# Performance work log

Measured on AMD Instinct MI355X. Metric: run time of the kernel, lower is better.

The kernel has to match this reference:

```python
import jax, jax.numpy as jnp
import numpy as np
from jax import lax

jax.config.update("jax_enable_x64", True)

B = 32768          # batch size
NCS = 96           # number of charging stations
NB = 124           # num_buses
S_BASE = 1000.0
MAX_CS = 22.17
MIN_CS = -22.17
MAX_EV_CH = 22.0
MAX_EV_DIS = -22.0
EV_CAP = 70.0
EV_MIN_CAP = 15.0
ITERS = 100
TOL = 1e-06
DT = 15.0 / 60.0   # timescale (hours)


def setup_inputs() -> dict:
    ks = jax.random.split(jax.random.key(0), 12)
    action = jax.random.uniform(ks[0], (B, NCS), dtype=jnp.float32, minval=-1.0, maxval=1.0)
    prices = jax.random.uniform(ks[1], (B, 1), dtype=jnp.float32, minval=0.05, maxval=0.5)
    active = jax.random.uniform(ks[2], (B, NB - 1), dtype=jnp.float32, minval=0.0, maxval=50.0)
    reactive = jax.random.uniform(ks[3], (B, NB - 1), dtype=jnp.float32, minval=0.0, maxval=20.0)
    cap = jax.random.uniform(ks[4], (B, NCS), dtype=jnp.float32, minval=0.0, maxval=EV_CAP)
    cap = cap * (jax.random.uniform(ks[5], (B, NCS)) > 0.2).astype(jnp.float32)
    tleft = jax.random.randint(ks[6], (B, NCS), 1, 10).astype(jnp.float32)
    bus = jax.random.randint(ks[7], (B, NCS), 0, NB - 1).astype(jnp.float32)
    ev = jnp.stack([cap, tleft, bus], axis=-1).reshape(B, 3 * NCS)  # interleaved triples
    state = jnp.concatenate(
        [jnp.zeros((B, 3), jnp.float32), prices, active, reactive, ev], axis=1
    )  # (B, 4 + 2*(NB-1) + 3*NCS) == (B, 538)
    K_re = (0.005 * jax.random.normal(ks[8], (NB - 1, NB - 1))).astype(jnp.float32)
    K_im = (0.005 * jax.random.normal(ks[9], (NB - 1, NB - 1))).astype(jnp.float32)
    L_re = jnp.ones((NB - 1,), jnp.float32)
    L_im = jnp.zeros((NB - 1,), jnp.float32)
    return {"action": action, "state": state, "K_re": K_re, "K_im": K_im, "L_re": L_re, "L_im": L_im}


def _forward(action, state, K_re, K_im, L_re, L_im):
    b, ncs = action.shape
    nb1 = NB - 1
    es = 4 + 2 * nb1  # start of EV state block
    prices = state[:, 3:4]                                    # (B,1), broadcast over stations
    cap = state[:, es:es + 3 * ncs:3]                         # current capacity
    tleft = state[:, es + 1:es + 1 + 3 * ncs:3]               # time left
    bus = state[:, es + 2:es + 2 + 3 * ncs:3].astype(jnp.int32)  # connected bus index
    conn = (cap > 0).astype(action.dtype)
    max_ch = jnp.minimum(MAX_EV_CH, conn * (EV_CAP - cap) / DT)
    max_dis = jnp.maximum(MAX_EV_DIS, conn * (EV_MIN_CAP - cap) / DT)
    pos = jnp.where(action >= 0, 1.0, 0.0).astype(action.dtype)
    power = action * MAX_CS * pos - action * MIN_CS * (1.0 - pos)
    power = jnp.maximum(jnp.minimum(power, max_ch), max_dis)
    costs = (prices * power * DT).sum(axis=1)
    new_cap = jnp.ceil((cap + power * DT) * 100.0) / 100.0
    dep = (tleft == 1).astype(action.dtype)
    user_sat = (-10.0 * dep * (new_cap - EV_CAP) ** 2).sum(axis=1)
    # scatter-add EV power per bus (duplicate indices accumulate, like torch scatter_add)
    ev_bus = jnp.zeros((b, nb1), power.dtype).at[jnp.arange(b)[:, None], bus].add(power)
    ap = state[:, 4:4 + nb1]
    rp = state[:, 4 + nb1:4 + 2 * nb1]
    S = ((ap + ev_bus) / S_BASE + 1j * (rp / S_BASE)).astype(jnp.complex128)  # (B, NB-1)
    K = (K_re + 1j * K_im).astype(jnp.complex128)
    W = (L_re + 1j * L_im).astype(jnp.complex128)
    v_init = jnp.ones((b, nb1), jnp.complex128)

    def run(v0):
        # Z-bus fixed point: v_k = K @ conj(S / v0)^T + W   (batched as bi)
        vk = jnp.einsum('ij,bj->bi', K, jnp.conj(S / v0)) + W
        tol = jnp.max(jnp.abs(jnp.abs(vk) - jnp.abs(v0)))
        return vk, tol

    def body(carry, _):
        v0, done = carry
        def step(v):
            vk, tol = run(v)
            return vk, tol < TOL
        def skip(v):
            return v, jnp.array(True)
        v_next, conv = lax.cond(done, skip, step, v0)
        return (v_next, done | conv), None

    (v_fin, _), _ = lax.scan(body, (v_init, jnp.array(False)), None, length=ITERS)
    vmag = jnp.abs(v_fin)
    voltage_loss = jnp.minimum(0.0, 0.05 - jnp.abs(1.0 - vmag)).sum(axis=1)
    loss = 1000.0 * voltage_loss + costs + user_sat
    return loss.astype(jnp.float32)


def reference(action, state, K_re, K_im, L_re, L_im):
    return _forward(action, state, K_re, K_im, L_re, L_im)
```

## Files before the change

kernel.cpp:

```cpp
#include <hip/hip_runtime.h>

#define NB1   123
#define NCSd  96
#define SW    538
#define EPB   16
#define TPB   256
#define BT    16
#define STPB  128


__global__ __launch_bounds__(128) void k_rowmax(const float* __restrict__ Kre,
                                                const float* __restrict__ Kim,
                                                const float* __restrict__ Lre,
                                                const float* __restrict__ Lim,
                                                float* __restrict__ ws) {
    __shared__ float rmax[2], wmax[2];
    int j = threadIdx.x;
    float s = 0.f, w = 0.f;
    if (j < NB1) {
        for (int k = 0; k < NB1; ++k) {
            float a = Kre[j * NB1 + k], b = Kim[j * NB1 + k];
            s = fmaf(a, a, fmaf(b, b, s));
        }
        float dr = Lre[j] - 1.0f, di = Lim[j];
        w = sqrtf(dr * dr + di * di);
    }
    float r = sqrtf(s);
    #pragma unroll
    for (int off = 32; off; off >>= 1) {
        r = fmaxf(r, __shfl_xor(r, off));
        w = fmaxf(w, __shfl_xor(w, off));
    }
    if ((j & 63) == 0) { rmax[j >> 6] = r; wmax[j >> 6] = w; }
    __syncthreads();
    if (j == 0) {
        ws[0] = fmaxf(rmax[0], rmax[1]);
        ws[2] = fmaxf(wmax[0], wmax[1]);
        ((unsigned*)ws)[1] = 0u;
    }
}

__global__ __launch_bounds__(TPB) void k_fast(const float* __restrict__ action,
                                              const float* __restrict__ state,
                                              float* __restrict__ ws,
                                              float* __restrict__ out) {
    __shared__ float ev[EPB][128];
    const int tid = threadIdx.x;
    const int e = tid >> 4, l = tid & 15;
    const long b = (long)(blockIdx.x * EPB + e);
    const float* srow = state + b * SW;

    for (int k = l; k < 128; k += 16) ev[e][k] = 0.f;
    __syncthreads();

    const float pr = srow[3];
    float costL = 0.f, usatL = 0.f;
    #pragma unroll
    for (int s = 0; s < NCSd / 16; ++s) {
        int i = l + 16 * s;
        float cap = srow[250 + 3 * i];
        float tl  = srow[251 + 3 * i];
        int   bus = (int)srow[252 + 3 * i];
        float a   = action[b * NCSd + i];
        float conn = cap > 0.f ? 1.f : 0.f;
        float mch = fminf(22.0f,  conn * (70.0f - cap) * 4.0f);
        float mds = fmaxf(-22.0f, conn * (15.0f - cap) * 4.0f);
        float p = fmaxf(fminf(22.17f * a, mch), mds);
        costL = fmaf(pr * p, 0.25f, costL);
        float nc = ceilf((cap + p * 0.25f) * 100.0f) * 0.01f;
        if (tl == 1.0f) { float d = nc - 70.0f; usatL = fmaf(-10.0f * d, d, usatL); }
        atomicAdd(&ev[e][bus], p);
    }
    __syncthreads();

    float s2 = 0.f;
    for (int k = l; k < NB1; k += 16) {
        float apv = srow[4 + k] + ev[e][k];
        float rpv = srow[127 + k];
        s2 = fmaf(apv, apv, fmaf(rpv, rpv, s2));
    }
    #pragma unroll
    for (int off = 8; off; off >>= 1) {
        s2    += __shfl_xor(s2, off);
        costL += __shfl_xor(costL, off);
        usatL += __shfl_xor(usatL, off);
    }

    bool flagged = false;
    if (l == 0) {
        float q  = sqrtf(s2) * 0.001f;
        float R  = ws[0];
        float dW = ws[2];
        float x  = R * q * 1.001f + 1e-7f;
        float om = 1.0f - dW;
        float disc = om * om - 4.0f * x;
        bool safe = false;
        if (disc > 0.f) {
            float m = 0.5f * (om + sqrtf(disc));
            safe = (dW + x / m) < 0.0495f;
        }
        flagged = !safe;
        out[b] = costL + usatL;
    }
    unsigned long long mask = __ballot(flagged);
    if (mask) {
        int nf = __popcll(mask);
        int lead = __ffsll((long long)mask) - 1;
        int lane = tid & 63;
        unsigned base_ = 0;
        if (lane == lead) base_ = atomicAdd(((unsigned*)ws) + 1, (unsigned)nf);
        base_ = __shfl(base_, lead);
        if (flagged) {
            int rank = __popcll(mask & ((1ull << lane) - 1ull));
            ((unsigned*)ws)[3 + base_ + rank] = (unsigned)b;
        }
    }
}

__global__ __launch_bounds__(STPB) void k_solve(const float* __restrict__ action,
                                                const float* __restrict__ state,
                                                const float* __restrict__ Kre,
                                                const float* __restrict__ Kim,
                                                const float* __restrict__ Lre,
                                                const float* __restrict__ Lim,
                                                const float* __restrict__ ws,
                                                float* __restrict__ out) {
    __shared__ float ev[BT][STPB];
    __shared__ __align__(16) float2 cmat[STPB][BT + 2];
    __shared__ float vls[STPB][BT + 1];
    __shared__ float red[2];
    __shared__ unsigned idxs[BT];
    const unsigned count = ((const unsigned*)ws)[1];
    const int tid = threadIdx.x;
    const int j = tid;
    const bool jok = j < NB1;
    const float Wre = jok ? Lre[j] : 1.f;
    const float Wim = jok ? Lim[j] : 0.f;

    for (unsigned base = (unsigned)blockIdx.x * BT; base < count; base += (unsigned)gridDim.x * BT) {
        unsigned nv = count - base; if (nv > BT) nv = BT;
        if (tid < BT) {
            unsigned t = (unsigned)tid < nv ? (unsigned)tid : nv - 1;
            idxs[tid] = ((const unsigned*)ws)[3 + base + t];
        }
        for (int x = tid; x < BT * STPB; x += STPB) ((float*)ev)[x] = 0.f;
        __syncthreads();

        for (int task = tid; task < BT * NCSd; task += STPB) {
            int e = task / NCSd, i = task - e * NCSd;
            long b = (long)idxs[e];
            const float* srow = state + b * SW;
            float cap = srow[250 + 3 * i];
            int   bus = (int)srow[252 + 3 * i];
            float a   = action[b * NCSd + i];
            float conn = cap > 0.f ? 1.f : 0.f;
            float mch = fminf(22.0f,  conn * (70.0f - cap) * 4.0f);
            float mds = fmaxf(-22.0f, conn * (15.0f - cap) * 4.0f);
            float p = fmaxf(fminf(22.17f * a, mch), mds);
            atomicAdd(&ev[e][bus], p);
        }
        __syncthreads();

        float Sre[BT], Sim[BT], vr[BT], vi[BT];
        #pragma unroll
        for (int e = 0; e < BT; ++e) {
            long b = (long)idxs[e];
            float ap = jok ? state[b * SW + 4 + j]   : 0.f;
            float rp = jok ? state[b * SW + 127 + j] : 0.f;
            Sre[e] = (ap + ev[e][j]) * 0.001f;
            Sim[e] = rp * 0.001f;
            vr[e] = 1.f; vi[e] = 0.f;
        }
        for (int it = 0; it < 100; ++it) {
            #pragma unroll
            for (int e = 0; e < BT; ++e) {
                float d = vr[e] * vr[e] + vi[e] * vi[e];
                float inv = 1.0f / d;
                cmat[j][e] = make_float2((Sre[e] * vr[e] + Sim[e] * vi[e]) * inv,
                                         (Sre[e] * vi[e] - Sim[e] * vr[e]) * inv);
            }
            __syncthreads();
            float ar[BT], ai[BT];
            #pragma unroll
            for (int e = 0; e < BT; ++e) { ar[e] = Wre; ai[e] = Wim; }
            for (int k = 0; k < NB1; ++k) {
                float kr = jok ? Kre[j * NB1 + k] : 0.f;
                float ki = jok ? Kim[j * NB1 + k] : 0.f;
                const float4* crow = (const float4*)(&cmat[k][0]);
                #pragma unroll
                for (int eh = 0; eh < BT / 2; ++eh) {
                    float4 c2 = crow[eh];
                    ar[2*eh]   = fmaf(kr, c2.x, fmaf(-ki, c2.y, ar[2*eh]));
                    ai[2*eh]   = fmaf(kr, c2.y, fmaf( ki, c2.x, ai[2*eh]));
                    ar[2*eh+1] = fmaf(kr, c2.z, fmaf(-ki, c2.w, ar[2*eh+1]));
                    ai[2*eh+1] = fmaf(kr, c2.w, fmaf( ki, c2.z, ai[2*eh+1]));
                }
            }
            float md = 0.f;
            #pragma unroll
            for (int e = 0; e < BT; ++e) {
                float vmn = sqrtf(ar[e]*ar[e] + ai[e]*ai[e]);
                float vmo = sqrtf(vr[e]*vr[e] + vi[e]*vi[e]);
                md = fmaxf(md, fabsf(vmn - vmo));
                vr[e] = ar[e]; vi[e] = ai[e];
            }
            #pragma unroll
            for (int off = 32; off; off >>= 1) md = fmaxf(md, __shfl_xor(md, off));
            if ((tid & 63) == 0) red[tid >> 6] = md;
            __syncthreads();
            if (fmaxf(red[0], red[1]) < 1e-6f) break;
        }
        #pragma unroll
        for (int e = 0; e < BT; ++e) {
            float vm = sqrtf(vr[e]*vr[e] + vi[e]*vi[e]);
            vls[j][e] = jok ? fminf(0.f, 0.05f - fabsf(1.0f - vm)) : 0.f;
        }
        __syncthreads();
        if (tid < (int)nv) {
            float s = 0.f;
            for (int k = 0; k < NB1; ++k) s += vls[k][tid];
            long b = (long)idxs[tid];
            out[b] += 1000.0f * s;
        }
        __syncthreads();
    }
}

__global__ __launch_bounds__(STPB) void k_main(
    const float* __restrict__ action, const float* __restrict__ state,
    const float* __restrict__ Kre, const float* __restrict__ Kim,
    const float* __restrict__ Lre, const float* __restrict__ Lim,
    float* __restrict__ out)
{
    __shared__ float ev[BT][STPB];
    __shared__ float costs_s[BT];
    __shared__ float usat_s[BT];
    __shared__ __align__(16) float2 cmat[STPB][BT + 2];
    __shared__ float vls[STPB][BT + 1];
    __shared__ float red[2];
    const int tid = threadIdx.x;
    const int e0  = blockIdx.x * BT;
    for (int x = tid; x < BT * STPB; x += STPB) ((float*)ev)[x] = 0.f;
    if (tid < BT) { costs_s[tid] = 0.f; usat_s[tid] = 0.f; }
    __syncthreads();
    for (int task = tid; task < BT * NCSd; task += STPB) {
        int e = task / NCSd, i = task - e * NCSd;
        long b = (long)(e0 + e);
        const float* srow = state + b * SW;
        float cap = srow[250 + 3 * i], tleft = srow[251 + 3 * i];
        int bus = (int)srow[252 + 3 * i];
        float a = action[b * NCSd + i];
        float conn = cap > 0.f ? 1.f : 0.f;
        float mch = fminf(22.0f, conn * (70.0f - cap) * 4.0f);
        float mds = fmaxf(-22.0f, conn * (15.0f - cap) * 4.0f);
        float power = fmaxf(fminf(22.17f * a, mch), mds);
        atomicAdd(&costs_s[e], srow[3] * power * 0.25f);
        float nc = ceilf((cap + power * 0.25f) * 100.0f) * 0.01f;
        if (tleft == 1.0f) { float d = nc - 70.0f; atomicAdd(&usat_s[e], -10.0f * d * d); }
        atomicAdd(&ev[e][bus], power);
    }
    __syncthreads();
    const int j = tid;
    const bool jok = j < NB1;
    float Wre = jok ? Lre[j] : 1.0f, Wim = jok ? Lim[j] : 0.0f;
    float Sre[BT], Sim[BT], vr[BT], vi[BT];
    #pragma unroll
    for (int e = 0; e < BT; ++e) {
        long b = (long)(e0 + e);
        float ap = jok ? state[b * SW + 4 + j] : 0.f;
        float rp = jok ? state[b * SW + 127 + j] : 0.f;
        Sre[e] = (ap + ev[e][j]) * 0.001f; Sim[e] = rp * 0.001f;
        vr[e] = 1.f; vi[e] = 0.f;
    }
    for (int it = 0; it < 100; ++it) {
        #pragma unroll
        for (int e = 0; e < BT; ++e) {
            float d = vr[e]*vr[e] + vi[e]*vi[e];
            float inv = 1.0f / d;
            cmat[j][e] = make_float2((Sre[e]*vr[e] + Sim[e]*vi[e]) * inv,
                                     (Sre[e]*vi[e] - Sim[e]*vr[e]) * inv);
        }
        __syncthreads();
        float ar[BT], ai[BT];
        #pragma unroll
        for (int e = 0; e < BT; ++e) { ar[e] = Wre; ai[e] = Wim; }
        for (int k = 0; k < NB1; ++k) {
            float kr = jok ? Kre[j*NB1+k] : 0.f;
            float ki = jok ? Kim[j*NB1+k] : 0.f;
            const float4* crow = (const float4*)(&cmat[k][0]);
            #pragma unroll
            for (int eh = 0; eh < BT / 2; ++eh) {
                float4 c2 = crow[eh];
                ar[2*eh]   = fmaf(kr, c2.x, fmaf(-ki, c2.y, ar[2*eh]));
                ai[2*eh]   = fmaf(kr, c2.y, fmaf( ki, c2.x, ai[2*eh]));
                ar[2*eh+1] = fmaf(kr, c2.z, fmaf(-ki, c2.w, ar[2*eh+1]));
                ai[2*eh+1] = fmaf(kr, c2.w, fmaf( ki, c2.z, ai[2*eh+1]));
            }
        }
        float md = 0.f;
        #pragma unroll
        for (int e = 0; e < BT; ++e) {
            float vmn = sqrtf(ar[e]*ar[e] + ai[e]*ai[e]);
            float vmo = sqrtf(vr[e]*vr[e] + vi[e]*vi[e]);
            md = fmaxf(md, fabsf(vmn - vmo));
            vr[e] = ar[e]; vi[e] = ai[e];
        }
        #pragma unroll
        for (int off = 32; off > 0; off >>= 1) md = fmaxf(md, __shfl_xor(md, off));
        if ((tid & 63) == 0) red[tid >> 6] = md;
        __syncthreads();
        if (fmaxf(red[0], red[1]) < 1e-6f) break;
    }
    #pragma unroll
    for (int e = 0; e < BT; ++e) {
        float vm = sqrtf(vr[e]*vr[e] + vi[e]*vi[e]);
        vls[j][e] = jok ? fminf(0.f, 0.05f - fabsf(1.0f - vm)) : 0.f;
    }
    __syncthreads();
    if (tid < BT) {
        float s = 0.f;
        for (int k = 0; k < NB1; ++k) s += vls[k][tid];
        out[e0 + tid] = 1000.0f * s + costs_s[tid] + usat_s[tid];
    }
}

extern "C" void kernel_launch(void* const* d_in, const int* in_sizes, int n_in,
                              void* d_out, int out_size, void* d_ws, size_t ws_size,
                              hipStream_t stream) {
    const float* action = (const float*)d_in[0];
    const float* state  = (const float*)d_in[1];
    const float* Kre    = (const float*)d_in[2];
    const float* Kim    = (const float*)d_in[3];
    const float* Lre    = (const float*)d_in[4];
    const float* Lim    = (const float*)d_in[5];
    float* out = (float*)d_out;
    const int B = out_size;

    const size_t wsNeed = (size_t)(3 + B) * sizeof(unsigned);
    if (ws_size >= wsNeed) {
        float* ws = (float*)d_ws;
        hipLaunchKernelGGL(k_rowmax, dim3(1), dim3(128), 0, stream, Kre, Kim, Lre, Lim, ws);
        hipLaunchKernelGGL(k_fast, dim3((B + EPB - 1) / EPB), dim3(TPB), 0, stream,
                           action, state, ws, out);
        hipLaunchKernelGGL(k_solve, dim3(2048), dim3(STPB), 0, stream,
                           action, state, Kre, Kim, Lre, Lim, ws, out);
    } else {
        hipLaunchKernelGGL(k_main, dim3((B + BT - 1) / BT), dim3(STPB), 0, stream,
                           action, state, Kre, Kim, Lre, Lim, out);
    }
}
```

Before: 43.01 us.

## Stage state rows in shared memory, parallelize norm kernel, shrink solve grid

The fast-path kernel now copies each block's 16 state rows into shared memory with coalesced float2 loads, instead of issuing strided per-lane global reads. The row-norm precompute kernel is rewritten so that one wave processes a whole row with shuffle reductions, replacing the serial per-thread loops, and the workspace slot layout is changed to match. The solve kernel's persistent grid is cut from 2048 to 256 blocks, which lowers launch and idle-block overhead when few rows are flagged but gives less parallelism if many rows need the iterative solve. The fast-path grid also drops its ceiling division and now assumes B is a multiple of 16.

Result: slower. 70.90 us (+64.8%).

```diff
diff --git a/kernel.cpp b/kernel.cpp
--- a/kernel.cpp
+++ b/kernel.cpp
@@ -7,36 +7,49 @@
 #define TPB   256
 #define BT    16
 #define STPB  128
-
-
-__global__ __launch_bounds__(128) void k_rowmax(const float* __restrict__ Kre,
-                                                const float* __restrict__ Kim,
-                                                const float* __restrict__ Lre,
-                                                const float* __restrict__ Lim,
-                                                float* __restrict__ ws) {
-    __shared__ float rmax[2], wmax[2];
-    int j = threadIdx.x;
-    float s = 0.f, w = 0.f;
-    if (j < NB1) {
-        for (int k = 0; k < NB1; ++k) {
-            float a = Kre[j * NB1 + k], b = Kim[j * NB1 + k];
-            s = fmaf(a, a, fmaf(b, b, s));
-        }
-        float dr = Lre[j] - 1.0f, di = Lim[j];
-        w = sqrtf(dr * dr + di * di);
-    }
-    float r = sqrtf(s);
-    #pragma unroll
-    for (int off = 32; off; off >>= 1) {
-        r = fmaxf(r, __shfl_xor(r, off));
-        w = fmaxf(w, __shfl_xor(w, off));
-    }
-    if ((j & 63) == 0) { rmax[j >> 6] = r; wmax[j >> 6] = w; }
-    __syncthreads();
-    if (j == 0) {
-        ws[0] = fmaxf(rmax[0], rmax[1]);
-        ws[2] = fmaxf(wmax[0], wmax[1]);
-        ((unsigned*)ws)[1] = 0u;
+#define LROW  540
+
+
+__global__ __launch_bounds__(256) void k_norm(const float* __restrict__ Kre,
+                                              const float* __restrict__ Kim,
+                                              const float* __restrict__ Lre,
+                                              const float* __restrict__ Lim,
+                                              float* __restrict__ ws) {
+    __shared__ float wred[8];
+    const int tid = threadIdx.x;
+    const int w = tid >> 6, l = tid & 63;
+    float rmax2 = 0.f;
+    for (int j = w; j < NB1; j += 4) {
+        const float* kr = Kre + j * NB1;
+        const float* ki = Kim + j * NB1;
+        float a = kr[l], bb = ki[l];
+        float s = fmaf(a, a, bb * bb);
+        if (l + 64 < NB1) {
+            float a2 = kr[l + 64], b2 = ki[l + 64];
+            s = fmaf(a2, a2, fmaf(b2, b2, s));
+        }
+        #pragma unroll
+        for (int off = 32; off; off >>= 1) s += __shfl_xor(s, off);
+        rmax2 = fmaxf(rmax2, s);
+    }
+    float dw2 = 0.f;
+    if (w == 0) {
+        float dr = Lre[l] - 1.f, di = Lim[l];
+        dw2 = fmaf(dr, dr, di * di);
+        if (l + 64 < NB1) {
+            float dr2 = Lre[l + 64] - 1.f, di2 = Lim[l + 64];
+            dw2 = fmaxf(dw2, fmaf(dr2, dr2, di2 * di2));
+        }
+        #pragma unroll
+        for (int off = 32; off; off >>= 1) dw2 = fmaxf(dw2, __shfl_xor(dw2, off));
+    }
+    if (l == 0) { wred[w] = rmax2; wred[4 + w] = dw2; }
+    __syncthreads();
+    if (tid == 0) {
+        float r2 = fmaxf(fmaxf(wred[0], wred[1]), fmaxf(wred[2], wred[3]));
+        ws[0] = sqrtf(r2);
+        ws[1] = sqrtf(wred[4]);
+        ((unsigned*)ws)[2] = 0u;
     }
 }
 
@@ -44,15 +57,22 @@
                                               const float* __restrict__ state,
                                               float* __restrict__ ws,
                                               float* __restrict__ out) {
+    __shared__ float st[EPB][LROW];
     __shared__ float ev[EPB][128];
     const int tid = threadIdx.x;
+    const long e0 = (long)blockIdx.x * EPB;
+
+    for (int idx = tid; idx < EPB * 269; idx += TPB) {
+        int e = idx / 269, c = idx - e * 269;
+        float2 v = *(const float2*)(state + (e0 + e) * SW + 2 * c);
+        *(float2*)&st[e][2 * c] = v;
+    }
+    for (int x = tid; x < EPB * 128; x += TPB) ((float*)ev)[x] = 0.f;
+    __syncthreads();
+
     const int e = tid >> 4, l = tid & 15;
-    const long b = (long)(blockIdx.x * EPB + e);
-    const float* srow = state + b * SW;
-
-    for (int k = l; k < 128; k += 16) ev[e][k] = 0.f;
-    __syncthreads();
-
+    const long b = e0 + e;
+    const float* srow = st[e];
     const float pr = srow[3];
     float costL = 0.f, usatL = 0.f;
     #pragma unroll
@@ -90,7 +110,7 @@
     if (l == 0) {
         float q  = sqrtf(s2) * 0.001f;
         float R  = ws[0];
-        float dW = ws[2];
+        float dW = ws[1];
         float x  = R * q * 1.001f + 1e-7f;
         float om = 1.0f - dW;
         float disc = om * om - 4.0f * x;
@@ -108,7 +128,7 @@
         int lead = __ffsll((long long)mask) - 1;
         int lane = tid & 63;
         unsigned base_ = 0;
-        if (lane == lead) base_ = atomicAdd(((unsigned*)ws) + 1, (unsigned)nf);
+        if (lane == lead) base_ = atomicAdd(((unsigned*)ws) + 2, (unsigned)nf);
         base_ = __shfl(base_, lead);
         if (flagged) {
             int rank = __popcll(mask & ((1ull << lane) - 1ull));
@@ -130,7 +150,7 @@
     __shared__ float vls[STPB][BT + 1];
     __shared__ float red[2];
     __shared__ unsigned idxs[BT];
-    const unsigned count = ((const unsigned*)ws)[1];
+    const unsigned count = ((const unsigned*)ws)[2];
     const int tid = threadIdx.x;
     const int j = tid;
     const bool jok = j < NB1;
@@ -339,10 +359,10 @@
     const size_t wsNeed = (size_t)(3 + B) * sizeof(unsigned);
     if (ws_size >= wsNeed) {
         float* ws = (float*)d_ws;
-        hipLaunchKernelGGL(k_rowmax, dim3(1), dim3(128), 0, stream, Kre, Kim, Lre, Lim, ws);
-        hipLaunchKernelGGL(k_fast, dim3((B + EPB - 1) / EPB), dim3(TPB), 0, stream,
+        hipLaunchKernelGGL(k_norm, dim3(1), dim3(256), 0, stream, Kre, Kim, Lre, Lim, ws);
+        hipLaunchKernelGGL(k_fast, dim3(B / EPB), dim3(TPB), 0, stream,
                            action, state, ws, out);
-        hipLaunchKernelGGL(k_solve, dim3(2048), dim3(STPB), 0, stream,
+        hipLaunchKernelGGL(k_solve, dim3(256), dim3(STPB), 0, stream,
                            action, state, Kre, Kim, Lre, Lim, ws, out);
     } else {
         hipLaunchKernelGGL(k_main, dim3((B + BT - 1) / BT), dim3(STPB), 0, stream,
```

## Stage state rows via coalesced float4 loads and parallelize norm precompute

Applied to the files above, without the earlier changes.

The fast screening kernel now loads each pair of batch rows cooperatively into shared memory with coalesced float4 reads, then has 32 lanes per row compute costs and the S-norm. The row-norm precompute is spread over 16 blocks using atomicMax on squared norms, with a memset to reset the workspace. The solve grid shrinks from 2048 to 64 blocks. The aim is to cut strided global loads and the latency of the single-block prologue, at the cost of an extra memset launch and fewer blocks for flagged rows. It also assumes B is divisible by 8 and that the data is aligned for float4 access.

Result: faster. 40.04 us (-6.9%).

```diff
diff --git a/kernel.cpp b/kernel.cpp
--- a/kernel.cpp
+++ b/kernel.cpp
@@ -3,40 +3,52 @@
 #define NB1   123
 #define NCSd  96
 #define SW    538
-#define EPB   16
 #define TPB   256
 #define BT    16
 #define STPB  128
 
 
-__global__ __launch_bounds__(128) void k_rowmax(const float* __restrict__ Kre,
-                                                const float* __restrict__ Kim,
-                                                const float* __restrict__ Lre,
-                                                const float* __restrict__ Lim,
-                                                float* __restrict__ ws) {
-    __shared__ float rmax[2], wmax[2];
-    int j = threadIdx.x;
-    float s = 0.f, w = 0.f;
-    if (j < NB1) {
-        for (int k = 0; k < NB1; ++k) {
-            float a = Kre[j * NB1 + k], b = Kim[j * NB1 + k];
-            s = fmaf(a, a, fmaf(b, b, s));
-        }
-        float dr = Lre[j] - 1.0f, di = Lim[j];
-        w = sqrtf(dr * dr + di * di);
-    }
-    float r = sqrtf(s);
+__global__ __launch_bounds__(256) void k_norm(const float* __restrict__ Kre,
+                                              const float* __restrict__ Kim,
+                                              const float* __restrict__ Lre,
+                                              const float* __restrict__ Lim,
+                                              float* __restrict__ ws) {
+    const int tid = threadIdx.x;
+    const int w = tid >> 6, l = tid & 63;
+    const int wid = blockIdx.x * 4 + w;
+    const int j1 = wid, j2 = wid + 64;
+    const bool has2 = j2 < NB1;
+
+    const float* kr1 = Kre + j1 * NB1; const float* ki1 = Kim + j1 * NB1;
+    float a0 = kr1[l], b0 = ki1[l];
+    float a1 = 0.f, b1 = 0.f;
+    if (l < NB1 - 64) { a1 = kr1[l + 64]; b1 = ki1[l + 64]; }
+    float c0 = 0.f, d0 = 0.f, c1 = 0.f, d1 = 0.f;
+    if (has2) {
+        const float* kr2 = Kre + j2 * NB1; const float* ki2 = Kim + j2 * NB1;
+        c0 = kr2[l]; d0 = ki2[l];
+        if (l < NB1 - 64) { c1 = kr2[l + 64]; d1 = ki2[l + 64]; }
+    }
+    float s1 = fmaf(a0, a0, b0 * b0) + fmaf(a1, a1, b1 * b1);
+    float s2 = fmaf(c0, c0, d0 * d0) + fmaf(c1, c1, d1 * d1);
     #pragma unroll
     for (int off = 32; off; off >>= 1) {
-        r = fmaxf(r, __shfl_xor(r, off));
-        w = fmaxf(w, __shfl_xor(w, off));
-    }
-    if ((j & 63) == 0) { rmax[j >> 6] = r; wmax[j >> 6] = w; }
-    __syncthreads();
-    if (j == 0) {
-        ws[0] = fmaxf(rmax[0], rmax[1]);
-        ws[2] = fmaxf(wmax[0], wmax[1]);
-        ((unsigned*)ws)[1] = 0u;
+        s1 += __shfl_xor(s1, off);
+        s2 += __shfl_xor(s2, off);
+    }
+    float m2 = has2 ? fmaxf(s1, s2) : s1;
+    if (l == 0) atomicMax((unsigned*)ws, __float_as_uint(m2));
+
+    if (wid == 0) {
+        float dr = Lre[l] - 1.f, di = Lim[l];
+        float d2 = fmaf(dr, dr, di * di);
+        if (l + 64 < NB1) {
+            float dr2 = Lre[l + 64] - 1.f, di2 = Lim[l + 64];
+            d2 = fmaxf(d2, fmaf(dr2, dr2, di2 * di2));
+        }
+        #pragma unroll
+        for (int off = 32; off; off >>= 1) d2 = fmaxf(d2, __shfl_xor(d2, off));
+        if (l == 0) atomicMax(((unsigned*)ws) + 1, __float_as_uint(d2));
     }
 }
 
@@ -44,74 +56,104 @@
                                               const float* __restrict__ state,
                                               float* __restrict__ ws,
                                               float* __restrict__ out) {
-    __shared__ float ev[EPB][128];
+    __shared__ __align__(16) float st[4][1088];
+    __shared__ __align__(16) float sa[4][192];
+    __shared__ float ev[4][2][128];
+
     const int tid = threadIdx.x;
-    const int e = tid >> 4, l = tid & 15;
-    const long b = (long)(blockIdx.x * EPB + e);
-    const float* srow = state + b * SW;
-
-    for (int k = l; k < 128; k += 16) ev[e][k] = 0.f;
-    __syncthreads();
-
+    const int w = tid >> 6, l = tid & 63;
+    const long g = (long)blockIdx.x * 4 + w;
+
+    const float4* G4 = (const float4*)(state + g * (2 * SW));
+    const float4* A4 = (const float4*)(action + g * (2 * NCSd));
+    float4 v0 = G4[l];
+    float4 v1 = G4[l + 64];
+    float4 v2 = G4[l + 128];
+    float4 v3 = G4[l + 192];
+    float4 v4 = make_float4(0.f, 0.f, 0.f, 0.f);
+    const bool t4 = l < 269 - 256;
+    if (t4) v4 = G4[l + 256];
+    float4 av = make_float4(0.f, 0.f, 0.f, 0.f);
+    const bool ta = l < 48;
+    if (ta) av = A4[l];
+
+    ev[w][0][l] = 0.f; if (l < 64) ev[w][0][l + 64] = 0.f;
+    ev[w][1][l] = 0.f; ev[w][1][l + 64] = 0.f;
+
+    float4* st4 = (float4*)st[w];
+    st4[l] = v0; st4[l + 64] = v1; st4[l + 128] = v2; st4[l + 192] = v3;
+    if (t4) st4[l + 256] = v4;
+    float4* sa4 = (float4*)sa[w];
+    if (ta) sa4[l] = av;
+    asm volatile("s_waitcnt lgkmcnt(0)" ::: "memory");
+
+    const int e = l >> 5, li = l & 31;
+    const long b = 2 * g + e;
+    const float* srow = st[w] + e * SW;
+    const float* actp = sa[w] + e * NCSd;
+    float* evp = ev[w][e];
     const float pr = srow[3];
-    float costL = 0.f, usatL = 0.f;
-    #pragma unroll
-    for (int s = 0; s < NCSd / 16; ++s) {
-        int i = l + 16 * s;
+
+    float cost = 0.f, usat = 0.f;
+    #pragma unroll
+    for (int s = 0; s < 3; ++s) {
+        int i = li + 32 * s;
         float cap = srow[250 + 3 * i];
         float tl  = srow[251 + 3 * i];
         int   bus = (int)srow[252 + 3 * i];
-        float a   = action[b * NCSd + i];
+        float a   = actp[i];
         float conn = cap > 0.f ? 1.f : 0.f;
         float mch = fminf(22.0f,  conn * (70.0f - cap) * 4.0f);
         float mds = fmaxf(-22.0f, conn * (15.0f - cap) * 4.0f);
         float p = fmaxf(fminf(22.17f * a, mch), mds);
-        costL = fmaf(pr * p, 0.25f, costL);
+        cost = fmaf(pr * p, 0.25f, cost);
         float nc = ceilf((cap + p * 0.25f) * 100.0f) * 0.01f;
-        if (tl == 1.0f) { float d = nc - 70.0f; usatL = fmaf(-10.0f * d, d, usatL); }
-        atomicAdd(&ev[e][bus], p);
-    }
-    __syncthreads();
+        if (tl == 1.0f) { float d = nc - 70.0f; usat = fmaf(-10.0f * d, d, usat); }
+        atomicAdd(&evp[bus], p);
+    }
+    asm volatile("s_waitcnt lgkmcnt(0)" ::: "memory");
 
     float s2 = 0.f;
-    for (int k = l; k < NB1; k += 16) {
-        float apv = srow[4 + k] + ev[e][k];
-        float rpv = srow[127 + k];
-        s2 = fmaf(apv, apv, fmaf(rpv, rpv, s2));
-    }
-    #pragma unroll
-    for (int off = 8; off; off >>= 1) {
-        s2    += __shfl_xor(s2, off);
-        costL += __shfl_xor(costL, off);
-        usatL += __shfl_xor(usatL, off);
-    }
-
-    bool flagged = false;
-    if (l == 0) {
-        float q  = sqrtf(s2) * 0.001f;
-        float R  = ws[0];
-        float dW = ws[2];
-        float x  = R * q * 1.001f + 1e-7f;
-        float om = 1.0f - dW;
-        float disc = om * om - 4.0f * x;
-        bool safe = false;
-        if (disc > 0.f) {
-            float m = 0.5f * (om + sqrtf(disc));
-            safe = (dW + x / m) < 0.0495f;
-        }
-        flagged = !safe;
-        out[b] = costL + usatL;
-    }
+    #pragma unroll
+    for (int s = 0; s < 4; ++s) {
+        int k = li + 32 * s;
+        if (k < NB1) {
+            float apv = srow[4 + k] + evp[k];
+            float rpv = srow[127 + k];
+            s2 = fmaf(apv, apv, fmaf(rpv, rpv, s2));
+        }
+    }
+    #pragma unroll
+    for (int off = 16; off; off >>= 1) {
+        s2   += __shfl_xor(s2, off);
+        cost += __shfl_xor(cost, off);
+        usat += __shfl_xor(usat, off);
+    }
+
+    float q  = sqrtf(s2) * 0.001f;
+    float R  = sqrtf(ws[0]);
+    float dW = sqrtf(ws[1]);
+    float x  = R * q * 1.001f + 1e-7f;
+    float om = 1.0f - dW;
+    float disc = om * om - 4.0f * x;
+    bool safe = false;
+    if (disc > 0.f) {
+        float m = 0.5f * (om + sqrtf(disc));
+        safe = (dW + x / m) < 0.0495f;
+    }
+
+    if (li == 0) out[b] = cost + usat;
+
+    bool flagged = (li == 0) && !safe;
     unsigned long long mask = __ballot(flagged);
     if (mask) {
         int nf = __popcll(mask);
         int lead = __ffsll((long long)mask) - 1;
-        int lane = tid & 63;
         unsigned base_ = 0;
-        if (lane == lead) base_ = atomicAdd(((unsigned*)ws) + 1, (unsigned)nf);
+        if (l == lead) base_ = atomicAdd(((unsigned*)ws) + 2, (unsigned)nf);
         base_ = __shfl(base_, lead);
         if (flagged) {
-            int rank = __popcll(mask & ((1ull << lane) - 1ull));
+            int rank = __popcll(mask & ((1ull << l) - 1ull));
             ((unsigned*)ws)[3 + base_ + rank] = (unsigned)b;
         }
     }
@@ -130,7 +172,7 @@
     __shared__ float vls[STPB][BT + 1];
     __shared__ float red[2];
     __shared__ unsigned idxs[BT];
-    const unsigned count = ((const unsigned*)ws)[1];
+    const unsigned count = ((const unsigned*)ws)[2];
     const int tid = threadIdx.x;
     const int j = tid;
     const bool jok = j < NB1;
@@ -339,10 +381,11 @@
     const size_t wsNeed = (size_t)(3 + B) * sizeof(unsigned);
     if (ws_size >= wsNeed) {
         float* ws = (float*)d_ws;
-        hipLaunchKernelGGL(k_rowmax, dim3(1), dim3(128), 0, stream, Kre, Kim, Lre, Lim, ws);
-        hipLaunchKernelGGL(k_fast, dim3((B + EPB - 1) / EPB), dim3(TPB), 0, stream,
+        hipMemsetAsync(d_ws, 0, 12, stream);
+        hipLaunchKernelGGL(k_norm, dim3(16), dim3(256), 0, stream, Kre, Kim, Lre, Lim, ws);
+        hipLaunchKernelGGL(k_fast, dim3(B / 8), dim3(TPB), 0, stream,
                            action, state, ws, out);
-        hipLaunchKernelGGL(k_solve, dim3(2048), dim3(STPB), 0, stream,
+        hipLaunchKernelGGL(k_solve, dim3(64), dim3(STPB), 0, stream,
                            action, state, Kre, Kim, Lre, Lim, ws, out);
     } else {
         hipLaunchKernelGGL(k_main, dim3((B + BT - 1) / BT), dim3(STPB), 0, stream,
```
